# Kernel optimization log

Measured on AMD Instinct MI355X. Metric: run time of the kernel, lower is better.

Reference implementation:

```python
import jax, jax.numpy as jnp
import numpy as np

N = 100000
E = 1600000
GENE = 512
HID = 128
NCLS = 10
EPS = 1e-5  # BatchNorm1d default eps


def setup_inputs() -> dict:
    key = jax.random.key(0)
    ks = jax.random.split(key, 16)
    def lin(k, fan_in, fan_out):
        return (jax.random.normal(k, (fan_in, fan_out), jnp.float32) / np.sqrt(fan_in)).astype(jnp.float32)
    dims = [(GENE, HID), (HID, 2 * HID), (2 * HID, HID), (HID, HID // 2)]
    inp = {}
    inp["x"] = jax.random.normal(ks[0], (N, GENE), jnp.float32)
    inp["edge_index"] = jax.random.randint(ks[1], (2, E), 0, N)
    for i, (di, do) in enumerate(dims, start=1):
        inp[f"W{i}"] = lin(ks[1 + i], di, do)
        inp[f"b{i}"] = jnp.zeros((do,), jnp.float32)
        inp[f"g{i}"] = jnp.ones((do,), jnp.float32)     # BN gamma
        inp[f"beta{i}"] = jnp.zeros((do,), jnp.float32)  # BN beta
    inp["Wc"] = lin(ks[10], HID // 2, NCLS)
    inp["bc"] = jnp.zeros((NCLS,), jnp.float32)
    return inp


def gcn_conv(h_in, W, b, src, dst, deg_inv_sqrt):
    # PyG GCNConv: transform, then symmetric-normalized aggregation with self-loops
    h = h_in @ W                                   # [N, out]
    norm = (deg_inv_sqrt[src] * deg_inv_sqrt[dst])[:, None]  # [E, 1]
    agg = jnp.zeros_like(h).at[dst].add(h[src] * norm)       # scatter-add over edges
    agg = agg + h * (deg_inv_sqrt ** 2)[:, None]   # self-loop contribution (norm = 1/deg)
    return agg + b


def relu_bn(h, g, beta):
    # forward applies BatchNorm1d(F.relu(h)) in training mode (batch stats, biased var)
    h = jax.nn.relu(h)
    mu = h.mean(axis=0)
    var = h.var(axis=0)
    return (h - mu) * jax.lax.rsqrt(var + EPS) * g + beta


def reference(x, edge_index, W1, b1, g1, beta1, W2, b2, g2, beta2,
              W3, b3, g3, beta3, W4, b4, g4, beta4, Wc, bc):
    src, dst = edge_index[0], edge_index[1]
    # degree after adding self-loops (edge weight 1)
    deg = jnp.zeros((x.shape[0],), x.dtype).at[dst].add(1.0) + 1.0
    dis = jax.lax.rsqrt(deg)
    h = relu_bn(gcn_conv(x, W1, b1, src, dst, dis), g1, beta1)
    h = relu_bn(gcn_conv(h, W2, b2, src, dst, dis), g2, beta2)
    h = relu_bn(gcn_conv(h, W3, b3, src, dst, dis), g3, beta3)
    h = relu_bn(gcn_conv(h, W4, b4, src, dst, dis), g4, beta4)
    return h @ Wc + bc
```

## Files before the change

kernel.cpp:

```cpp
#include <hip/hip_runtime.h>
#include <hip/hip_bf16.h>

#define EPS_BN 1e-5f

using frag8 = __attribute__((ext_vector_type(8))) short;
using f32x4 = __attribute__((ext_vector_type(4))) float;

typedef const __attribute__((address_space(1))) void* gas_ptr;
typedef __attribute__((address_space(3))) void* las_ptr;

__device__ __forceinline__ void async_ld16(const void* g, void* l) {
  __builtin_amdgcn_global_load_lds((gas_ptr)g, (las_ptr)l, 16, 0, 0);
}

__device__ __forceinline__ float bfu2f(unsigned short u) {
  union { unsigned int i; float f; } c;
  c.i = (unsigned int)u << 16;
  return c.f;
}

__global__ __launch_bounds__(256) void prep_fat_kernel(
    const int* __restrict__ e_dst, int* __restrict__ cnt, int* __restrict__ rank, int E,
    int CB,
    const float* __restrict__ x, __hip_bfloat16* __restrict__ Xb, size_t n4, int VB,
    const float* __restrict__ W1, const float* __restrict__ W2,
    const float* __restrict__ W3, const float* __restrict__ W4,
    __hip_bfloat16* __restrict__ T1, __hip_bfloat16* __restrict__ T2,
    __hip_bfloat16* __restrict__ T3, __hip_bfloat16* __restrict__ T4) {
  int b = (int)blockIdx.x;
  int tid = (int)threadIdx.x;
  if (b < CB) {
    int e = b * 256 + tid;
    if (e < E) rank[e] = atomicAdd(&cnt[e_dst[e]], 1);
  } else if (b < CB + VB) {
    size_t i = (size_t)(b - CB) * 256 + tid;
    size_t stride = (size_t)VB * 256;
    for (; i < n4; i += stride) {
      float4 v = *(const float4*)&x[i * 4];
      union { ushort4 u; __hip_bfloat16 h[4]; } pk;
      pk.h[0] = __float2bfloat16(v.x);
      pk.h[1] = __float2bfloat16(v.y);
      pk.h[2] = __float2bfloat16(v.z);
      pk.h[3] = __float2bfloat16(v.w);
      *(ushort4*)&Xb[i * 4] = pk.u;
    }
  } else {
    int i = (b - CB - VB) * 256 + tid;
    const float* W; __hip_bfloat16* T; int F, K, base;
    if (i < 65536)        { W = W1; T = T1; K = 512; F = 128; base = 0; }
    else if (i < 98304)   { W = W2; T = T2; K = 128; F = 256; base = 65536; }
    else if (i < 131072)  { W = W3; T = T3; K = 256; F = 128; base = 98304; }
    else if (i < 139264)  { W = W4; T = T4; K = 128; F = 64;  base = 131072; }
    else return;
    int j = i - base;
    int k = j / F, f = j % F;
    T[f * K + k] = __float2bfloat16(W[j]);
  }
}

__global__ void scan1_kernel(const int* __restrict__ cnt, int* __restrict__ out,
                             int* __restrict__ bsum, float* __restrict__ dis, int n) {
  __shared__ int sdata[1024];
  int tid = threadIdx.x;
  int i = blockIdx.x * 1024 + tid;
  int v = (i < n) ? cnt[i] : 0;
  if (i < n) dis[i] = rsqrtf((float)v + 1.0f);
  sdata[tid] = v;
  __syncthreads();
  for (int off = 1; off < 1024; off <<= 1) {
    int t = (tid >= off) ? sdata[tid - off] : 0;
    __syncthreads();
    sdata[tid] += t;
    __syncthreads();
  }
  if (i < n) out[i] = sdata[tid] - v;
  if (tid == 1023) bsum[blockIdx.x] = sdata[1023];
}

__global__ void scan2_kernel(int* __restrict__ bsum, int nb) {
  __shared__ int sdata[1024];
  int tid = threadIdx.x;
  int v = (tid < nb) ? bsum[tid] : 0;
  sdata[tid] = v;
  __syncthreads();
  for (int off = 1; off < 1024; off <<= 1) {
    int t = (tid >= off) ? sdata[tid - off] : 0;
    __syncthreads();
    sdata[tid] += t;
    __syncthreads();
  }
  if (tid < nb) bsum[tid] = sdata[tid] - v;
}

__global__ void scan3_kernel(int* __restrict__ out, const int* __restrict__ bsum,
                             int n, int E) {
  int i = blockIdx.x * 1024 + threadIdx.x;
  if (i < n) out[i] += bsum[blockIdx.x];
  if (i == 0) out[n] = E;
}

template <int TN, int OMODE>
__device__ __forceinline__ void gemm_body(
    const __hip_bfloat16* __restrict__ A, const __hip_bfloat16* __restrict__ Bt,
    void* __restrict__ Cv, const float* __restrict__ bias,
    const float* __restrict__ rowscale, float* __restrict__ stats,
    int Nr, int K, int F, int bx, int by) {
  constexpr int WM = (TN == 128) ? 64 : 32;
  constexpr int MI = WM / 16;
  __shared__ __align__(16) __hip_bfloat16 As[128 * 32];
  __shared__ __align__(16) __hip_bfloat16 Bs[TN * 32];
  __shared__ float sacc[128], sqc[128];
  int tid = (int)threadIdx.x;
  int wid = tid >> 6, lane = tid & 63;
  int rowBase = bx * 128;
  int colBase = by * TN;
  int wr, wc;
  if (TN == 128) { wr = (wid >> 1) * 64; wc = (wid & 1) * 64; }
  else           { wr = wid * 32;        wc = 0; }

  f32x4 zero = {0.f, 0.f, 0.f, 0.f};
  f32x4 acc[MI][4];
#pragma unroll
  for (int i = 0; i < MI; ++i)
#pragma unroll
    for (int j = 0; j < 4; ++j) acc[i][j] = zero;

  int lm = lane & 15;
  int k8 = (lane >> 4) * 8;

  if constexpr (OMODE == 2) {
    if (tid < 128) { sacc[tid] = 0.f; sqc[tid] = 0.f; }
  }

  for (int k0 = 0; k0 < K; k0 += 32) {
#pragma unroll
    for (int p = 0; p < 2; ++p) {
      int sidx = p * 256 + tid;
      int row = sidx >> 2;
      int kq = (sidx & 3) * 8;
      int gr = rowBase + row;
      if (gr >= Nr) gr = Nr - 1;
      async_ld16(A + (size_t)gr * K + k0 + kq, (char*)As + (p * 256 + wid * 64) * 16);
    }
    constexpr int BPASS = TN / 64;
#pragma unroll
    for (int p = 0; p < BPASS; ++p) {
      int sidx = p * 256 + tid;
      int col = sidx >> 2;
      int kq = (sidx & 3) * 8;
      async_ld16(Bt + (size_t)(colBase + col) * K + k0 + kq,
                 (char*)Bs + (p * 256 + wid * 64) * 16);
    }
    __syncthreads();

    frag8 af[MI], bf[4];
#pragma unroll
    for (int i = 0; i < MI; ++i)
      af[i] = *(const frag8*)&As[(wr + i * 16 + lm) * 32 + k8];
#pragma unroll
    for (int j = 0; j < 4; ++j)
      bf[j] = *(const frag8*)&Bs[(wc + j * 16 + lm) * 32 + k8];
#pragma unroll
    for (int i = 0; i < MI; ++i)
#pragma unroll
      for (int j = 0; j < 4; ++j)
        acc[i][j] = __builtin_amdgcn_mfma_f32_16x16x32_bf16(af[i], bf[j], acc[i][j], 0, 0, 0);
    __syncthreads();
  }

  int rquad = (lane >> 4) * 4;
  float s[4] = {0.f, 0.f, 0.f, 0.f}, q[4] = {0.f, 0.f, 0.f, 0.f};
#pragma unroll
  for (int i = 0; i < MI; ++i) {
    int rb = rowBase + wr + i * 16 + rquad;
#pragma unroll
    for (int r = 0; r < 4; ++r) {
      int row = rb + r;
      if (row < Nr) {
        if constexpr (OMODE == 1) {
          float rs = rowscale[row];
#pragma unroll
          for (int j = 0; j < 4; ++j) {
            int col = colBase + wc + j * 16 + lm;
            ((__hip_bfloat16*)Cv)[(size_t)row * F + col] = __float2bfloat16(acc[i][j][r] * rs);
          }
        } else {
#pragma unroll
          for (int j = 0; j < 4; ++j) {
            int col = colBase + wc + j * 16 + lm;
            float v = acc[i][j][r] + bias[col];
            ((float*)Cv)[(size_t)row * F + col] = v;
            float rl = fmaxf(v, 0.f);
            s[j] += rl;
            q[j] += rl * rl;
          }
        }
      }
    }
  }

  if constexpr (OMODE == 2) {
#pragma unroll
    for (int j = 0; j < 4; ++j) {
      s[j] += __shfl_xor(s[j], 16, 64); s[j] += __shfl_xor(s[j], 32, 64);
      q[j] += __shfl_xor(q[j], 16, 64); q[j] += __shfl_xor(q[j], 32, 64);
    }
    if (lane < 16) {
#pragma unroll
      for (int j = 0; j < 4; ++j) {
        atomicAdd(&sacc[wc + j * 16 + lane], s[j]);
        atomicAdd(&sqc[wc + j * 16 + lane], q[j]);
      }
    }
    __syncthreads();
    if (tid < 128) {
      atomicAdd(&stats[colBase + tid], sacc[tid]);
      atomicAdd(&stats[256 + colBase + tid], sqc[tid]);
    }
  }
}

template <int TN, int OMODE>
__global__ __launch_bounds__(256) void mfma_gemm_kernel(
    const __hip_bfloat16* __restrict__ A, const __hip_bfloat16* __restrict__ Bt,
    void* __restrict__ Cv, const float* __restrict__ bias,
    const float* __restrict__ rowscale, float* __restrict__ stats,
    int Nr, int K, int F) {
  gemm_body<TN, OMODE>(A, Bt, Cv, bias, rowscale, stats, Nr, K, F,
                       (int)blockIdx.x, (int)blockIdx.y);
}

__global__ __launch_bounds__(256) void gemm1_scatter_kernel(
    const __hip_bfloat16* __restrict__ A, const __hip_bfloat16* __restrict__ Bt,
    void* __restrict__ Cv, const float* __restrict__ rowscale,
    int Nr, int K, int F, int G1,
    const int* __restrict__ src, const int* __restrict__ dst,
    const int* __restrict__ rowstart, const int* __restrict__ rank,
    int* __restrict__ csr_src, int E) {
  int b = (int)blockIdx.x;
  if (b < G1) {
    gemm_body<128, 1>(A, Bt, Cv, nullptr, rowscale, nullptr, Nr, K, F, b, 0);
  } else {
    int e = (b - G1) * 256 + (int)threadIdx.x;
    if (e < E) csr_src[rowstart[dst[e]] + rank[e]] = src[e];
  }
}

template <int VEC, int OMODE>
__global__ __launch_bounds__(256) void agg_kernel(
    const __hip_bfloat16* __restrict__ Ts, const int* __restrict__ rowstart,
    const int* __restrict__ csr_src, const float* __restrict__ dis,
    const float* __restrict__ bias, void* __restrict__ H,
    float* __restrict__ stats, int Nn, int F) {
  __shared__ float lsum[512], lqs[512];
  int tid = (int)threadIdx.x;
  int wid4 = tid >> 6;
  int lane = tid & 63;
  int off = lane * VEC;
  const unsigned short* Tu = (const unsigned short*)Ts;

  float bj[VEC];
  float s[VEC], q[VEC];
#pragma unroll
  for (int j = 0; j < VEC; ++j) {
    bj[j] = (OMODE == 1) ? bias[off + j] : 0.f;
    s[j] = 0.f; q[j] = 0.f;
  }

  for (int d = blockIdx.x * 4 + wid4; d < Nn; d += gridDim.x * 4) {
    float acc[VEC];
    {
      unsigned short r[VEC];
      if constexpr (VEC == 2) *(ushort2*)r = *(const ushort2*)&Tu[(size_t)d * F + off];
      else                    r[0] = Tu[(size_t)d * F + off];
#pragma unroll
      for (int j = 0; j < VEC; ++j) acc[j] = bfu2f(r[j]);
    }

    int e0 = rowstart[d], e1 = rowstart[d + 1];
    for (int e = e0; e < e1; e += 16) {
      int idx[16];
      bool val[16];
#pragma unroll
      for (int p = 0; p < 16; ++p) {
        int ee = e + p;
        val[p] = ee < e1;
        idx[p] = csr_src[val[p] ? ee : e1 - 1];
      }
      unsigned short r[16][VEC];
#pragma unroll
      for (int p = 0; p < 16; ++p) {
        if constexpr (VEC == 2) *(ushort2*)r[p] = *(const ushort2*)&Tu[(size_t)idx[p] * F + off];
        else                    r[p][0] = Tu[(size_t)idx[p] * F + off];
      }
#pragma unroll
      for (int p = 0; p < 16; ++p)
#pragma unroll
        for (int j = 0; j < VEC; ++j) acc[j] += val[p] ? bfu2f(r[p][j]) : 0.f;
    }

    float dd = dis[d];
    if constexpr (OMODE == 0) {
      union { ushort2 u; __hip_bfloat16 h[2]; } pk;
      if constexpr (VEC == 2) {
        pk.h[0] = __float2bfloat16(acc[0] * dd);
        pk.h[1] = __float2bfloat16(acc[1] * dd);
        *(ushort2*)&((__hip_bfloat16*)H)[(size_t)d * F + off] = pk.u;
      } else {
        ((__hip_bfloat16*)H)[(size_t)d * F + off] = __float2bfloat16(acc[0] * dd);
      }
    } else {
      float v[VEC];
#pragma unroll
      for (int j = 0; j < VEC; ++j) {
        v[j] = acc[j] * dd + bj[j];
        float rl = fmaxf(v[j], 0.f);
        s[j] += rl;
        q[j] += rl * rl;
      }
      if constexpr (VEC == 2) {
        *(float2*)&((float*)H)[(size_t)d * F + off] = make_float2(v[0], v[1]);
      } else {
        ((float*)H)[(size_t)d * F + off] = v[0];
      }
    }
  }

  if constexpr (OMODE == 1) {
#pragma unroll
    for (int j = 0; j < VEC; ++j) {
      lsum[(lane * VEC + j) * 4 + wid4] = s[j];
      lqs[(lane * VEC + j) * 4 + wid4] = q[j];
    }
    __syncthreads();
    int nc = 64 * VEC;
    for (int c = tid; c < nc; c += 256) {
      float a = lsum[c * 4 + 0] + lsum[c * 4 + 1] + lsum[c * 4 + 2] + lsum[c * 4 + 3];
      float b = lqs[c * 4 + 0] + lqs[c * 4 + 1] + lqs[c * 4 + 2] + lqs[c * 4 + 3];
      atomicAdd(&stats[c], a);
      atomicAdd(&stats[256 + c], b);
    }
  }
}

__global__ __launch_bounds__(256) void bnapply_kernel(
    const float* __restrict__ H, const float* __restrict__ stats,
    const float* __restrict__ g, const float* __restrict__ beta,
    const float* __restrict__ rowscale, __hip_bfloat16* __restrict__ O,
    size_t total4, int F, int logF, float invN) {
  __shared__ float ssc[256], ssb[256];
  int tid = (int)threadIdx.x;
  if (tid < F) {
    float mean = stats[tid] * invN;
    float var = stats[256 + tid] * invN - mean * mean;
    float sc = g[tid] * rsqrtf(var + EPS_BN);
    ssc[tid] = sc;
    ssb[tid] = beta[tid] - mean * sc;
  }
  __syncthreads();
  size_t i = (size_t)blockIdx.x * blockDim.x + tid;
  size_t stride = (size_t)gridDim.x * blockDim.x;
  for (; i < total4; i += stride) {
    size_t b = i * 4;
    float4 v = *(const float4*)&H[b];
    int c = (int)(b & (size_t)(F - 1));
    float rs = rowscale ? rowscale[b >> logF] : 1.0f;
    union { ushort4 u; __hip_bfloat16 h[4]; } pk;
    pk.h[0] = __float2bfloat16((fmaxf(v.x, 0.f) * ssc[c + 0] + ssb[c + 0]) * rs);
    pk.h[1] = __float2bfloat16((fmaxf(v.y, 0.f) * ssc[c + 1] + ssb[c + 1]) * rs);
    pk.h[2] = __float2bfloat16((fmaxf(v.z, 0.f) * ssc[c + 2] + ssb[c + 2]) * rs);
    pk.h[3] = __float2bfloat16((fmaxf(v.w, 0.f) * ssc[c + 3] + ssb[c + 3]) * rs);
    *(ushort4*)&O[b] = pk.u;
  }
}

__global__ __launch_bounds__(256) void bnapply_cls_kernel(
    const float* __restrict__ Hf, const float* __restrict__ stats,
    const float* __restrict__ g, const float* __restrict__ beta,
    const float* __restrict__ Wc, const float* __restrict__ bc,
    float* __restrict__ out, int Nn, float invN) {
  __shared__ float ssc[64], ssb[64];
  int tid = (int)threadIdx.x;
  if (tid < 64) {
    float mean = stats[tid] * invN;
    float var = stats[256 + tid] * invN - mean * mean;
    float sc = g[tid] * rsqrtf(var + EPS_BN);
    ssc[tid] = sc;
    ssb[tid] = beta[tid] - mean * sc;
  }
  __syncthreads();
  int gt = blockIdx.x * blockDim.x + tid;
  int wid = gt >> 6;
  int lane = tid & 63;
  if (wid >= Nn) return;
  float v = Hf[(size_t)wid * 64 + lane];
  float h = fmaxf(v, 0.f) * ssc[lane] + ssb[lane];
#pragma unroll
  for (int c = 0; c < 10; ++c) {
    float p = h * Wc[lane * 10 + c];
#pragma unroll
    for (int off = 32; off > 0; off >>= 1) p += __shfl_down(p, off, 64);
    if (lane == 0) out[(size_t)wid * 10 + c] = p + bc[c];
  }
}


extern "C" void kernel_launch(void* const* d_in, const int* in_sizes, int n_in,
                              void* d_out, int out_size, void* d_ws, size_t ws_size,
                              hipStream_t stream) {
  (void)n_in; (void)out_size; (void)ws_size;
  const float* x    = (const float*)d_in[0];
  const int*   edge = (const int*)d_in[1];
  const int E  = in_sizes[1] / 2;
  const int Nn = in_sizes[0] / 512;
  const int* e_src = edge;
  const int* e_dst = edge + E;

  const float* W[4]  = {(const float*)d_in[2],  (const float*)d_in[6],
                        (const float*)d_in[10], (const float*)d_in[14]};
  const float* bv[4] = {(const float*)d_in[3],  (const float*)d_in[7],
                        (const float*)d_in[11], (const float*)d_in[15]};
  const float* gv[4] = {(const float*)d_in[4],  (const float*)d_in[8],
                        (const float*)d_in[12], (const float*)d_in[16]};
  const float* bt[4] = {(const float*)d_in[5],  (const float*)d_in[9],
                        (const float*)d_in[13], (const float*)d_in[17]};
  const float* Wc = (const float*)d_in[18];
  const float* bc = (const float*)d_in[19];
  float* out = (float*)d_out;

  const int Kdim[4] = {512, 128, 256, 128};
  const int Fdim[4] = {128, 256, 128, 64};
  const float invN = 1.0f / (float)Nn;

  char* p = (char*)d_ws;
  auto alloc = [&](size_t bytes) -> void* {
    void* r = (void*)p;
    p += (bytes + 255) & ~(size_t)255;
    return r;
  };
  int*   cnt      = (int*)alloc((size_t)Nn * 4);
  float* stats    = (float*)alloc(2048 * 4);
  size_t zeroBytes = (size_t)(((size_t)Nn * 4 + 255) & ~(size_t)255) + 2048 * 4;
  int*   rowstart = (int*)alloc((size_t)(Nn + 1) * 4);
  int*   bsum     = (int*)alloc(1024 * 4);
  float* dis      = (float*)alloc((size_t)Nn * 4);
  int*   rank     = (int*)alloc((size_t)E * 4);
  int*   csr_src  = (int*)alloc((size_t)E * 4);
  __hip_bfloat16* Wt[4];
  for (int l = 0; l < 4; ++l)
    Wt[l] = (__hip_bfloat16*)alloc((size_t)Kdim[l] * Fdim[l] * 2);
  char* R0 = (char*)alloc((size_t)Nn * 512 * 2);
  __hip_bfloat16* Tb = (__hip_bfloat16*)alloc((size_t)Nn * 256 * 2);
  __hip_bfloat16* P0 = (__hip_bfloat16*)alloc((size_t)Nn * 256 * 2);
  __hip_bfloat16* P1 = (__hip_bfloat16*)alloc((size_t)Nn * 256 * 2);
  __hip_bfloat16* Xb = (__hip_bfloat16*)R0;
  float*          Hf = (float*)R0;

  hipMemsetAsync(cnt, 0, zeroBytes, stream);

  const int CB = (E + 255) / 256;
  const int VB = 2048;
  const int WB = (139264 + 255) / 256;
  prep_fat_kernel<<<CB + VB + WB, 256, 0, stream>>>(
      e_dst, cnt, rank, E, CB,
      x, Xb, (size_t)Nn * 512 / 4, VB,
      W[0], W[1], W[2], W[3], Wt[0], Wt[1], Wt[2], Wt[3]);

  int nb = (Nn + 1023) / 1024;
  scan1_kernel<<<nb, 1024, 0, stream>>>(cnt, rowstart, bsum, dis, Nn);
  scan2_kernel<<<1, 1024, 0, stream>>>(bsum, nb);
  scan3_kernel<<<nb, 1024, 0, stream>>>(rowstart, bsum, Nn, E);

  const int AGG_BLOCKS = 1536;
  int gx = (Nn + 127) / 128;

  gemm1_scatter_kernel<<<gx + CB, 256, 0, stream>>>(
      Xb, Wt[0], Tb, dis, Nn, 512, 128, gx,
      e_src, e_dst, rowstart, rank, csr_src, E);
  agg_kernel<2, 1><<<AGG_BLOCKS, 256, 0, stream>>>(Tb, rowstart, csr_src, dis,
                                                   bv[0], Hf, stats, Nn, 128);
  bnapply_kernel<<<(int)(((size_t)Nn * 128 / 4 + 255) / 256), 256, 0, stream>>>(
      Hf, stats, gv[0], bt[0], dis, P0, (size_t)Nn * 128 / 4, 128, 7, invN);

  agg_kernel<2, 0><<<AGG_BLOCKS, 256, 0, stream>>>(P0, rowstart, csr_src, dis,
                                                   nullptr, Tb, nullptr, Nn, 128);
  {
    dim3 g(gx, 2);
    mfma_gemm_kernel<128, 2><<<g, 256, 0, stream>>>(Tb, Wt[1], Hf, bv[1], nullptr,
                                                    stats + 512, Nn, 128, 256);
  }
  bnapply_kernel<<<(int)(((size_t)Nn * 256 / 4 + 255) / 256), 256, 0, stream>>>(
      Hf, stats + 512, gv[1], bt[1], nullptr, P1, (size_t)Nn * 256 / 4, 256, 8, invN);

  {
    dim3 g(gx, 1);
    mfma_gemm_kernel<128, 1><<<g, 256, 0, stream>>>(P1, Wt[2], Tb, nullptr, dis, nullptr,
                                                    Nn, 256, 128);
  }
  agg_kernel<2, 1><<<AGG_BLOCKS, 256, 0, stream>>>(Tb, rowstart, csr_src, dis,
                                                   bv[2], Hf, stats + 1024, Nn, 128);
  bnapply_kernel<<<(int)(((size_t)Nn * 128 / 4 + 255) / 256), 256, 0, stream>>>(
      Hf, stats + 1024, gv[2], bt[2], nullptr, P0, (size_t)Nn * 128 / 4, 128, 7, invN);

  {
    dim3 g(gx, 1);
    mfma_gemm_kernel<64, 1><<<g, 256, 0, stream>>>(P0, Wt[3], Tb, nullptr, dis, nullptr,
                                                   Nn, 128, 64);
  }
  agg_kernel<1, 1><<<AGG_BLOCKS, 256, 0, stream>>>(Tb, rowstart, csr_src, dis,
                                                   bv[3], Hf, stats + 1536, Nn, 64);
  int clsBlocks = (Nn * 64 + 255) / 256;
  bnapply_cls_kernel<<<clsBlocks, 256, 0, stream>>>(Hf, stats + 1536, gv[3], bt[3],
                                                    Wc, bc, out, Nn, invN);
}
```

Baseline: 1.040 ms.

## Fuse BatchNorm apply into aggregation and GEMM loaders, drop standalone BN passes

Removes the separate bnapply kernels by folding the BN affine transform into the next consumer: the layer-2 aggregation uses a per-node sum of neighbour norms so the affine can be applied after summation, and the GEMM A-loaders apply scale and shift while staging tiles. Layer 1 now reads fp32 x directly in the GEMM, with an in-register bf16 conversion, instead of a separate conversion pass. Row scaling by dis is moved into a fused scatter kernel. Intermediates are stored as bf16 ReLU outputs rather than fp32 pre-activations. This cuts memory traffic and launch count, but the synchronous A-loads replace async LDS loads and the GEMM runs before the CSR build, which changes rounding and the overlap pattern.

```diff
diff --git a/kernel.cpp b/kernel.cpp
--- a/kernel.cpp
+++ b/kernel.cpp
@@ -19,42 +19,12 @@
   return c.f;
 }
 
-__global__ __launch_bounds__(256) void prep_fat_kernel(
-    const int* __restrict__ e_dst, int* __restrict__ cnt, int* __restrict__ rank, int E,
-    int CB,
-    const float* __restrict__ x, __hip_bfloat16* __restrict__ Xb, size_t n4, int VB,
-    const float* __restrict__ W1, const float* __restrict__ W2,
-    const float* __restrict__ W3, const float* __restrict__ W4,
-    __hip_bfloat16* __restrict__ T1, __hip_bfloat16* __restrict__ T2,
-    __hip_bfloat16* __restrict__ T3, __hip_bfloat16* __restrict__ T4) {
-  int b = (int)blockIdx.x;
-  int tid = (int)threadIdx.x;
-  if (b < CB) {
-    int e = b * 256 + tid;
-    if (e < E) rank[e] = atomicAdd(&cnt[e_dst[e]], 1);
-  } else if (b < CB + VB) {
-    size_t i = (size_t)(b - CB) * 256 + tid;
-    size_t stride = (size_t)VB * 256;
-    for (; i < n4; i += stride) {
-      float4 v = *(const float4*)&x[i * 4];
-      union { ushort4 u; __hip_bfloat16 h[4]; } pk;
-      pk.h[0] = __float2bfloat16(v.x);
-      pk.h[1] = __float2bfloat16(v.y);
-      pk.h[2] = __float2bfloat16(v.z);
-      pk.h[3] = __float2bfloat16(v.w);
-      *(ushort4*)&Xb[i * 4] = pk.u;
-    }
-  } else {
-    int i = (b - CB - VB) * 256 + tid;
-    const float* W; __hip_bfloat16* T; int F, K, base;
-    if (i < 65536)        { W = W1; T = T1; K = 512; F = 128; base = 0; }
-    else if (i < 98304)   { W = W2; T = T2; K = 128; F = 256; base = 65536; }
-    else if (i < 131072)  { W = W3; T = T3; K = 256; F = 128; base = 98304; }
-    else if (i < 139264)  { W = W4; T = T4; K = 128; F = 64;  base = 131072; }
-    else return;
-    int j = i - base;
-    int k = j / F, f = j % F;
-    T[f * K + k] = __float2bfloat16(W[j]);
+
+__global__ void wtrans1_kernel(const float* __restrict__ W1, __hip_bfloat16* __restrict__ T) {
+  int i = blockIdx.x * blockDim.x + threadIdx.x;
+  if (i < 512 * 128) {
+    int k = i / 128, f = i % 128;
+    T[f * 512 + k] = __float2bfloat16(W1[i]);
   }
 }
 
@@ -99,17 +69,20 @@
   if (i == 0) out[n] = E;
 }
 
-template <int TN, int OMODE>
+template <int TN, int ASTAGE, int OMODE>
 __device__ __forceinline__ void gemm_body(
-    const __hip_bfloat16* __restrict__ A, const __hip_bfloat16* __restrict__ Bt,
-    void* __restrict__ Cv, const float* __restrict__ bias,
-    const float* __restrict__ rowscale, float* __restrict__ stats,
+    const void* __restrict__ Ap, const __hip_bfloat16* __restrict__ Bt,
+    __hip_bfloat16* __restrict__ C, const float* __restrict__ bias,
+    const float* __restrict__ rowscale,
+    const float* __restrict__ statsIn, const float* __restrict__ g,
+    const float* __restrict__ beta, float* __restrict__ statsOut, float invN,
     int Nr, int K, int F, int bx, int by) {
   constexpr int WM = (TN == 128) ? 64 : 32;
   constexpr int MI = WM / 16;
   __shared__ __align__(16) __hip_bfloat16 As[128 * 32];
   __shared__ __align__(16) __hip_bfloat16 Bs[TN * 32];
   __shared__ float sacc[128], sqc[128];
+  __shared__ float ssc[256], ssb[256];
   int tid = (int)threadIdx.x;
   int wid = tid >> 6, lane = tid & 63;
   int rowBase = bx * 128;
@@ -128,19 +101,65 @@
   int lm = lane & 15;
   int k8 = (lane >> 4) * 8;
 
-  if constexpr (OMODE == 2) {
+  if constexpr (OMODE == 3) {
     if (tid < 128) { sacc[tid] = 0.f; sqc[tid] = 0.f; }
   }
+  if constexpr (ASTAGE == 2) {
+    for (int k = tid; k < K; k += 256) {
+      float mean = statsIn[k] * invN;
+      float var = statsIn[256 + k] * invN - mean * mean;
+      float sc = g[k] * rsqrtf(var + EPS_BN);
+      ssc[k] = sc;
+      ssb[k] = beta[k] - mean * sc;
+    }
+    __syncthreads();
+  }
 
   for (int k0 = 0; k0 < K; k0 += 32) {
-#pragma unroll
-    for (int p = 0; p < 2; ++p) {
-      int sidx = p * 256 + tid;
-      int row = sidx >> 2;
-      int kq = (sidx & 3) * 8;
-      int gr = rowBase + row;
-      if (gr >= Nr) gr = Nr - 1;
-      async_ld16(A + (size_t)gr * K + k0 + kq, (char*)As + (p * 256 + wid * 64) * 16);
+    if constexpr (ASTAGE == 0) {
+#pragma unroll
+      for (int p = 0; p < 2; ++p) {
+        int sidx = p * 256 + tid;
+        int row = sidx >> 2;
+        int kq = (sidx & 3) * 8;
+        int gr = rowBase + row;
+        if (gr >= Nr) gr = Nr - 1;
+        async_ld16((const __hip_bfloat16*)Ap + (size_t)gr * K + k0 + kq,
+                   (char*)As + (p * 256 + wid * 64) * 16);
+      }
+    } else {
+#pragma unroll
+      for (int p = 0; p < 2; ++p) {
+        int sidx = p * 256 + tid;
+        int row = sidx >> 2;
+        int kq = (sidx & 3) * 8;
+        int gr = rowBase + row;
+        if (gr >= Nr) gr = Nr - 1;
+        union { frag8 f; __hip_bfloat16 h[8]; } pk;
+        if constexpr (ASTAGE == 1) {
+          const float* s = (const float*)Ap + (size_t)gr * K + k0 + kq;
+          float4 a = *(const float4*)s;
+          float4 b2 = *(const float4*)(s + 4);
+          pk.h[0] = __float2bfloat16(a.x);  pk.h[1] = __float2bfloat16(a.y);
+          pk.h[2] = __float2bfloat16(a.z);  pk.h[3] = __float2bfloat16(a.w);
+          pk.h[4] = __float2bfloat16(b2.x); pk.h[5] = __float2bfloat16(b2.y);
+          pk.h[6] = __float2bfloat16(b2.z); pk.h[7] = __float2bfloat16(b2.w);
+        } else {
+          const unsigned short* s = (const unsigned short*)Ap + (size_t)gr * K + k0 + kq;
+          ushort4 a = *(const ushort4*)s;
+          ushort4 b2 = *(const ushort4*)(s + 4);
+          int kk = k0 + kq;
+          pk.h[0] = __float2bfloat16(bfu2f(a.x)  * ssc[kk + 0] + ssb[kk + 0]);
+          pk.h[1] = __float2bfloat16(bfu2f(a.y)  * ssc[kk + 1] + ssb[kk + 1]);
+          pk.h[2] = __float2bfloat16(bfu2f(a.z)  * ssc[kk + 2] + ssb[kk + 2]);
+          pk.h[3] = __float2bfloat16(bfu2f(a.w)  * ssc[kk + 3] + ssb[kk + 3]);
+          pk.h[4] = __float2bfloat16(bfu2f(b2.x) * ssc[kk + 4] + ssb[kk + 4]);
+          pk.h[5] = __float2bfloat16(bfu2f(b2.y) * ssc[kk + 5] + ssb[kk + 5]);
+          pk.h[6] = __float2bfloat16(bfu2f(b2.z) * ssc[kk + 6] + ssb[kk + 6]);
+          pk.h[7] = __float2bfloat16(bfu2f(b2.w) * ssc[kk + 7] + ssb[kk + 7]);
+        }
+        *(frag8*)&As[row * 32 + kq] = pk.f;
+      }
     }
     constexpr int BPASS = TN / 64;
 #pragma unroll
@@ -177,20 +196,26 @@
     for (int r = 0; r < 4; ++r) {
       int row = rb + r;
       if (row < Nr) {
-        if constexpr (OMODE == 1) {
-          float rs = rowscale[row];
+        if constexpr (OMODE == 0) {
 #pragma unroll
           for (int j = 0; j < 4; ++j) {
             int col = colBase + wc + j * 16 + lm;
-            ((__hip_bfloat16*)Cv)[(size_t)row * F + col] = __float2bfloat16(acc[i][j][r] * rs);
+            C[(size_t)row * F + col] = __float2bfloat16(acc[i][j][r]);
+          }
+        } else if constexpr (OMODE == 1) {
+          float rs = rowscale[row];
+#pragma unroll
+          for (int j = 0; j < 4; ++j) {
+            int col = colBase + wc + j * 16 + lm;
+            C[(size_t)row * F + col] = __float2bfloat16(acc[i][j][r] * rs);
           }
         } else {
 #pragma unroll
           for (int j = 0; j < 4; ++j) {
             int col = colBase + wc + j * 16 + lm;
             float v = acc[i][j][r] + bias[col];
-            ((float*)Cv)[(size_t)row * F + col] = v;
             float rl = fmaxf(v, 0.f);
+            C[(size_t)row * F + col] = __float2bfloat16(rl);
             s[j] += rl;
             q[j] += rl * rl;
           }
@@ -199,7 +224,7 @@
     }
   }
 
-  if constexpr (OMODE == 2) {
+  if constexpr (OMODE == 3) {
 #pragma unroll
     for (int j = 0; j < 4; ++j) {
       s[j] += __shfl_xor(s[j], 16, 64); s[j] += __shfl_xor(s[j], 32, 64);
@@ -214,56 +239,114 @@
     }
     __syncthreads();
     if (tid < 128) {
-      atomicAdd(&stats[colBase + tid], sacc[tid]);
-      atomicAdd(&stats[256 + colBase + tid], sqc[tid]);
-    }
-  }
-}
-
-template <int TN, int OMODE>
+      atomicAdd(&statsOut[colBase + tid], sacc[tid]);
+      atomicAdd(&statsOut[256 + colBase + tid], sqc[tid]);
+    }
+  }
+}
+
+__global__ __launch_bounds__(256) void fat1_kernel(
+    const float* __restrict__ x, const __hip_bfloat16* __restrict__ Wt0,
+    __hip_bfloat16* __restrict__ T1, int Nn, int G1,
+    const int* __restrict__ e_dst, int* __restrict__ cnt, int* __restrict__ rank,
+    int E, int CB,
+    const float* __restrict__ W2, const float* __restrict__ W3, const float* __restrict__ W4,
+    __hip_bfloat16* __restrict__ Tw2, __hip_bfloat16* __restrict__ Tw3,
+    __hip_bfloat16* __restrict__ Tw4) {
+  int b = (int)blockIdx.x;
+  if (b < G1) {
+    gemm_body<128, 1, 0>(x, Wt0, T1, nullptr, nullptr, nullptr, nullptr, nullptr,
+                         nullptr, 0.f, Nn, 512, 128, b, 0);
+  } else if (b < G1 + CB) {
+    int e = (b - G1) * 256 + (int)threadIdx.x;
+    if (e < E) rank[e] = atomicAdd(&cnt[e_dst[e]], 1);
+  } else {
+    int i = (b - G1 - CB) * 256 + (int)threadIdx.x;
+    const float* W; __hip_bfloat16* T; int K, F, base;
+    if (i < 32768)       { W = W2; T = Tw2; K = 128; F = 256; base = 0; }
+    else if (i < 65536)  { W = W3; T = Tw3; K = 256; F = 128; base = 32768; }
+    else if (i < 73728)  { W = W4; T = Tw4; K = 128; F = 64;  base = 65536; }
+    else return;
+    int j = i - base;
+    int k = j / F, f = j % F;
+    T[f * K + k] = __float2bfloat16(W[j]);
+  }
+}
+
+template <int TN, int ASTAGE, int OMODE>
 __global__ __launch_bounds__(256) void mfma_gemm_kernel(
-    const __hip_bfloat16* __restrict__ A, const __hip_bfloat16* __restrict__ Bt,
-    void* __restrict__ Cv, const float* __restrict__ bias,
-    const float* __restrict__ rowscale, float* __restrict__ stats,
-    int Nr, int K, int F) {
-  gemm_body<TN, OMODE>(A, Bt, Cv, bias, rowscale, stats, Nr, K, F,
-                       (int)blockIdx.x, (int)blockIdx.y);
-}
-
-__global__ __launch_bounds__(256) void gemm1_scatter_kernel(
-    const __hip_bfloat16* __restrict__ A, const __hip_bfloat16* __restrict__ Bt,
-    void* __restrict__ Cv, const float* __restrict__ rowscale,
-    int Nr, int K, int F, int G1,
+    const void* __restrict__ A, const __hip_bfloat16* __restrict__ Bt,
+    __hip_bfloat16* __restrict__ C, const float* __restrict__ bias,
+    const float* __restrict__ rowscale, const float* __restrict__ statsIn,
+    const float* __restrict__ g, const float* __restrict__ beta,
+    float* __restrict__ statsOut, float invN, int Nr, int K, int F) {
+  gemm_body<TN, ASTAGE, OMODE>(A, Bt, C, bias, rowscale, statsIn, g, beta, statsOut,
+                               invN, Nr, K, F, (int)blockIdx.x, (int)blockIdx.y);
+}
+
+__global__ __launch_bounds__(256) void fat2_kernel(
     const int* __restrict__ src, const int* __restrict__ dst,
     const int* __restrict__ rowstart, const int* __restrict__ rank,
-    int* __restrict__ csr_src, int E) {
+    int* __restrict__ csr_src, int E, int SB,
+    __hip_bfloat16* __restrict__ T1, const float* __restrict__ dis, int n8) {
   int b = (int)blockIdx.x;
-  if (b < G1) {
-    gemm_body<128, 1>(A, Bt, Cv, nullptr, rowscale, nullptr, Nr, K, F, b, 0);
+  if (b < SB) {
+    int e = b * 256 + (int)threadIdx.x;
+    if (e < E) csr_src[rowstart[dst[e]] + rank[e]] = src[e];
   } else {
-    int e = (b - G1) * 256 + (int)threadIdx.x;
-    if (e < E) csr_src[rowstart[dst[e]] + rank[e]] = src[e];
-  }
-}
-
-template <int VEC, int OMODE>
+    int i = (b - SB) * 256 + (int)threadIdx.x;
+    if (i < n8) {
+      float dd = dis[i >> 4];
+      unsigned short* p8 = (unsigned short*)T1 + (size_t)i * 8;
+      ushort4 a = *(ushort4*)p8;
+      ushort4 c = *(ushort4*)(p8 + 4);
+      union { ushort4 u; __hip_bfloat16 h[4]; } o0, o1;
+      o0.h[0] = __float2bfloat16(bfu2f(a.x) * dd);
+      o0.h[1] = __float2bfloat16(bfu2f(a.y) * dd);
+      o0.h[2] = __float2bfloat16(bfu2f(a.z) * dd);
+      o0.h[3] = __float2bfloat16(bfu2f(a.w) * dd);
+      o1.h[0] = __float2bfloat16(bfu2f(c.x) * dd);
+      o1.h[1] = __float2bfloat16(bfu2f(c.y) * dd);
+      o1.h[2] = __float2bfloat16(bfu2f(c.z) * dd);
+      o1.h[3] = __float2bfloat16(bfu2f(c.w) * dd);
+      *(ushort4*)p8 = o0.u;
+      *(ushort4*)(p8 + 4) = o1.u;
+    }
+  }
+}
+
+template <int VEC, int AMODE>
 __global__ __launch_bounds__(256) void agg_kernel(
     const __hip_bfloat16* __restrict__ Ts, const int* __restrict__ rowstart,
     const int* __restrict__ csr_src, const float* __restrict__ dis,
     const float* __restrict__ bias, void* __restrict__ H,
-    float* __restrict__ stats, int Nn, int F) {
+    float* __restrict__ stats, const float* __restrict__ statsIn,
+    const float* __restrict__ g, const float* __restrict__ beta,
+    float* __restrict__ sd, float invN, int Nn, int F) {
   __shared__ float lsum[512], lqs[512];
+  __shared__ float ssc[128], ssb[128];
   int tid = (int)threadIdx.x;
   int wid4 = tid >> 6;
   int lane = tid & 63;
   int off = lane * VEC;
   const unsigned short* Tu = (const unsigned short*)Ts;
 
+  if constexpr (AMODE == 2) {
+    if (tid < F) {
+      float mean = statsIn[tid] * invN;
+      float var = statsIn[256 + tid] * invN - mean * mean;
+      float sc = g[tid] * rsqrtf(var + EPS_BN);
+      ssc[tid] = sc;
+      ssb[tid] = beta[tid] - mean * sc;
+    }
+    __syncthreads();
+  }
+
   float bj[VEC];
   float s[VEC], q[VEC];
 #pragma unroll
   for (int j = 0; j < VEC; ++j) {
-    bj[j] = (OMODE == 1) ? bias[off + j] : 0.f;
+    bj[j] = (AMODE == 1 || AMODE == 3 || AMODE == 4) ? bias[off + j] : 0.f;
     s[j] = 0.f; q[j] = 0.f;
   }
 
@@ -276,6 +359,8 @@
 #pragma unroll
       for (int j = 0; j < VEC; ++j) acc[j] = bfu2f(r[j]);
     }
+    float dd = dis[d];
+    float sdacc = dd;
 
     int e0 = rowstart[d], e1 = rowstart[d + 1];
     for (int e = e0; e < e1; e += 16) {
@@ -288,45 +373,54 @@
         idx[p] = csr_src[val[p] ? ee : e1 - 1];
       }
       unsigned short r[16][VEC];
+      float dv[16];
 #pragma unroll
       for (int p = 0; p < 16; ++p) {
         if constexpr (VEC == 2) *(ushort2*)r[p] = *(const ushort2*)&Tu[(size_t)idx[p] * F + off];
         else                    r[p][0] = Tu[(size_t)idx[p] * F + off];
-      }
-#pragma unroll
-      for (int p = 0; p < 16; ++p)
+        if constexpr (AMODE == 1) dv[p] = dis[idx[p]];
+      }
+#pragma unroll
+      for (int p = 0; p < 16; ++p) {
 #pragma unroll
         for (int j = 0; j < VEC; ++j) acc[j] += val[p] ? bfu2f(r[p][j]) : 0.f;
-    }
-
-    float dd = dis[d];
-    if constexpr (OMODE == 0) {
+        if constexpr (AMODE == 1) sdacc += val[p] ? dv[p] : 0.f;
+      }
+    }
+
+    if constexpr (AMODE == 2) {
+      float sdv = sd[d];
       union { ushort2 u; __hip_bfloat16 h[2]; } pk;
-      if constexpr (VEC == 2) {
-        pk.h[0] = __float2bfloat16(acc[0] * dd);
-        pk.h[1] = __float2bfloat16(acc[1] * dd);
+      pk.h[0] = __float2bfloat16(dd * (ssc[off + 0] * acc[0] + ssb[off + 0] * sdv));
+      pk.h[1] = __float2bfloat16(dd * (ssc[off + 1] * acc[1] + ssb[off + 1] * sdv));
+      *(ushort2*)&((__hip_bfloat16*)H)[(size_t)d * F + off] = pk.u;
+    } else {
+      float rl[VEC];
+#pragma unroll
+      for (int j = 0; j < VEC; ++j) {
+        float v = acc[j] * dd + bj[j];
+        rl[j] = fmaxf(v, 0.f);
+        s[j] += rl[j];
+        q[j] += rl[j] * rl[j];
+      }
+      if constexpr (AMODE == 1) {
+        union { ushort2 u; __hip_bfloat16 h[2]; } pk;
+        pk.h[0] = __float2bfloat16(rl[0] * dd);
+        pk.h[1] = __float2bfloat16(rl[1] * dd);
+        *(ushort2*)&((__hip_bfloat16*)H)[(size_t)d * F + off] = pk.u;
+        if (lane == 0) sd[d] = sdacc;
+      } else if constexpr (AMODE == 3) {
+        union { ushort2 u; __hip_bfloat16 h[2]; } pk;
+        pk.h[0] = __float2bfloat16(rl[0]);
+        pk.h[1] = __float2bfloat16(rl[1]);
         *(ushort2*)&((__hip_bfloat16*)H)[(size_t)d * F + off] = pk.u;
       } else {
-        ((__hip_bfloat16*)H)[(size_t)d * F + off] = __float2bfloat16(acc[0] * dd);
-      }
-    } else {
-      float v[VEC];
-#pragma unroll
-      for (int j = 0; j < VEC; ++j) {
-        v[j] = acc[j] * dd + bj[j];
-        float rl = fmaxf(v[j], 0.f);
-        s[j] += rl;
-        q[j] += rl * rl;
-      }
-      if constexpr (VEC == 2) {
-        *(float2*)&((float*)H)[(size_t)d * F + off] = make_float2(v[0], v[1]);
-      } else {
-        ((float*)H)[(size_t)d * F + off] = v[0];
-      }
-    }
-  }
-
-  if constexpr (OMODE == 1) {
+        ((float*)H)[(size_t)d * F + off] = rl[0];
+      }
+    }
+  }
+
+  if constexpr (AMODE != 2) {
 #pragma unroll
     for (int j = 0; j < VEC; ++j) {
       lsum[(lane * VEC + j) * 4 + wid4] = s[j];
@@ -343,39 +437,8 @@
   }
 }
 
-__global__ __launch_bounds__(256) void bnapply_kernel(
-    const float* __restrict__ H, const float* __restrict__ stats,
-    const float* __restrict__ g, const float* __restrict__ beta,
-    const float* __restrict__ rowscale, __hip_bfloat16* __restrict__ O,
-    size_t total4, int F, int logF, float invN) {
-  __shared__ float ssc[256], ssb[256];
-  int tid = (int)threadIdx.x;
-  if (tid < F) {
-    float mean = stats[tid] * invN;
-    float var = stats[256 + tid] * invN - mean * mean;
-    float sc = g[tid] * rsqrtf(var + EPS_BN);
-    ssc[tid] = sc;
-    ssb[tid] = beta[tid] - mean * sc;
-  }
-  __syncthreads();
-  size_t i = (size_t)blockIdx.x * blockDim.x + tid;
-  size_t stride = (size_t)gridDim.x * blockDim.x;
-  for (; i < total4; i += stride) {
-    size_t b = i * 4;
-    float4 v = *(const float4*)&H[b];
-    int c = (int)(b & (size_t)(F - 1));
-    float rs = rowscale ? rowscale[b >> logF] : 1.0f;
-    union { ushort4 u; __hip_bfloat16 h[4]; } pk;
-    pk.h[0] = __float2bfloat16((fmaxf(v.x, 0.f) * ssc[c + 0] + ssb[c + 0]) * rs);
-    pk.h[1] = __float2bfloat16((fmaxf(v.y, 0.f) * ssc[c + 1] + ssb[c + 1]) * rs);
-    pk.h[2] = __float2bfloat16((fmaxf(v.z, 0.f) * ssc[c + 2] + ssb[c + 2]) * rs);
-    pk.h[3] = __float2bfloat16((fmaxf(v.w, 0.f) * ssc[c + 3] + ssb[c + 3]) * rs);
-    *(ushort4*)&O[b] = pk.u;
-  }
-}
-
 __global__ __launch_bounds__(256) void bnapply_cls_kernel(
-    const float* __restrict__ Hf, const float* __restrict__ stats,
+    const float* __restrict__ R4, const float* __restrict__ stats,
     const float* __restrict__ g, const float* __restrict__ beta,
     const float* __restrict__ Wc, const float* __restrict__ bc,
     float* __restrict__ out, int Nn, float invN) {
@@ -393,8 +456,8 @@
   int wid = gt >> 6;
   int lane = tid & 63;
   if (wid >= Nn) return;
-  float v = Hf[(size_t)wid * 64 + lane];
-  float h = fmaxf(v, 0.f) * ssc[lane] + ssb[lane];
+  float v = R4[(size_t)wid * 64 + lane];
+  float h = v * ssc[lane] + ssb[lane];
 #pragma unroll
   for (int c = 0; c < 10; ++c) {
     float p = h * Wc[lane * 10 + c];
@@ -428,8 +491,6 @@
   const float* bc = (const float*)d_in[19];
   float* out = (float*)d_out;
 
-  const int Kdim[4] = {512, 128, 256, 128};
-  const int Fdim[4] = {128, 256, 128, 64};
   const float invN = 1.0f / (float)Nn;
 
   char* p = (char*)d_ws;
@@ -444,72 +505,76 @@
   int*   rowstart = (int*)alloc((size_t)(Nn + 1) * 4);
   int*   bsum     = (int*)alloc(1024 * 4);
   float* dis      = (float*)alloc((size_t)Nn * 4);
+  float* sd       = (float*)alloc((size_t)Nn * 4);
   int*   rank     = (int*)alloc((size_t)E * 4);
   int*   csr_src  = (int*)alloc((size_t)E * 4);
-  __hip_bfloat16* Wt[4];
-  for (int l = 0; l < 4; ++l)
-    Wt[l] = (__hip_bfloat16*)alloc((size_t)Kdim[l] * Fdim[l] * 2);
-  char* R0 = (char*)alloc((size_t)Nn * 512 * 2);
-  __hip_bfloat16* Tb = (__hip_bfloat16*)alloc((size_t)Nn * 256 * 2);
-  __hip_bfloat16* P0 = (__hip_bfloat16*)alloc((size_t)Nn * 256 * 2);
-  __hip_bfloat16* P1 = (__hip_bfloat16*)alloc((size_t)Nn * 256 * 2);
-  __hip_bfloat16* Xb = (__hip_bfloat16*)R0;
-  float*          Hf = (float*)R0;
+  __hip_bfloat16* Wt0 = (__hip_bfloat16*)alloc(512 * 128 * 2);
+  __hip_bfloat16* Wt1 = (__hip_bfloat16*)alloc(128 * 256 * 2);
+  __hip_bfloat16* Wt2 = (__hip_bfloat16*)alloc(256 * 128 * 2);
+  __hip_bfloat16* Wt3 = (__hip_bfloat16*)alloc(128 * 64 * 2);
+  __hip_bfloat16* Ts1 = (__hip_bfloat16*)alloc((size_t)Nn * 128 * 2);
+  __hip_bfloat16* R1  = (__hip_bfloat16*)alloc((size_t)Nn * 128 * 2);
+  __hip_bfloat16* Tb2 = (__hip_bfloat16*)alloc((size_t)Nn * 128 * 2);
+  __hip_bfloat16* R2  = (__hip_bfloat16*)alloc((size_t)Nn * 256 * 2);
+  __hip_bfloat16* Ts3 = (__hip_bfloat16*)alloc((size_t)Nn * 128 * 2);
+  __hip_bfloat16* R3  = (__hip_bfloat16*)alloc((size_t)Nn * 128 * 2);
+  __hip_bfloat16* Ts4 = (__hip_bfloat16*)alloc((size_t)Nn * 64 * 2);
+  float*          R4  = (float*)alloc((size_t)Nn * 64 * 4);
 
   hipMemsetAsync(cnt, 0, zeroBytes, stream);
 
+  wtrans1_kernel<<<(512 * 128 + 255) / 256, 256, 0, stream>>>(W[0], Wt0);
+
+  const int gx = (Nn + 127) / 128;
   const int CB = (E + 255) / 256;
-  const int VB = 2048;
-  const int WB = (139264 + 255) / 256;
-  prep_fat_kernel<<<CB + VB + WB, 256, 0, stream>>>(
-      e_dst, cnt, rank, E, CB,
-      x, Xb, (size_t)Nn * 512 / 4, VB,
-      W[0], W[1], W[2], W[3], Wt[0], Wt[1], Wt[2], Wt[3]);
+  const int WB = (73728 + 255) / 256;
+  fat1_kernel<<<gx + CB + WB, 256, 0, stream>>>(
+      x, Wt0, Ts1, Nn, gx, e_dst, cnt, rank, E, CB,
+      W[1], W[2], W[3], Wt1, Wt2, Wt3);
 
   int nb = (Nn + 1023) / 1024;
   scan1_kernel<<<nb, 1024, 0, stream>>>(cnt, rowstart, bsum, dis, Nn);
   scan2_kernel<<<1, 1024, 0, stream>>>(bsum, nb);
   scan3_kernel<<<nb, 1024, 0, stream>>>(rowstart, bsum, Nn, E);
 
-  const int AGG_BLOCKS = 1536;
-  int gx = (Nn + 127) / 128;
-
-  gemm1_scatter_kernel<<<gx + CB, 256, 0, stream>>>(
-      Xb, Wt[0], Tb, dis, Nn, 512, 128, gx,
-      e_src, e_dst, rowstart, rank, csr_src, E);
-  agg_kernel<2, 1><<<AGG_BLOCKS, 256, 0, stream>>>(Tb, rowstart, csr_src, dis,
-                                                   bv[0], Hf, stats, Nn, 128);
-  bnapply_kernel<<<(int)(((size_t)Nn * 128 / 4 + 255) / 256), 256, 0, stream>>>(
-      Hf, stats, gv[0], bt[0], dis, P0, (size_t)Nn * 128 / 4, 128, 7, invN);
-
-  agg_kernel<2, 0><<<AGG_BLOCKS, 256, 0, stream>>>(P0, rowstart, csr_src, dis,
-                                                   nullptr, Tb, nullptr, Nn, 128);
+  int n8 = Nn * 128 / 8;
+  int TB = (n8 + 255) / 256;
+  fat2_kernel<<<CB + TB, 256, 0, stream>>>(e_src, e_dst, rowstart, rank, csr_src, E, CB,
+                                           Ts1, dis, n8);
+
+  const int AGG_BLOCKS = 2048;
+
+  agg_kernel<2, 1><<<AGG_BLOCKS, 256, 0, stream>>>(
+      Ts1, rowstart, csr_src, dis, bv[0], R1, stats, nullptr, nullptr, nullptr,
+      sd, invN, Nn, 128);
+  agg_kernel<2, 2><<<AGG_BLOCKS, 256, 0, stream>>>(
+      R1, rowstart, csr_src, dis, nullptr, Tb2, nullptr, stats, gv[0], bt[0],
+      sd, invN, Nn, 128);
   {
     dim3 g(gx, 2);
-    mfma_gemm_kernel<128, 2><<<g, 256, 0, stream>>>(Tb, Wt[1], Hf, bv[1], nullptr,
-                                                    stats + 512, Nn, 128, 256);
-  }
-  bnapply_kernel<<<(int)(((size_t)Nn * 256 / 4 + 255) / 256), 256, 0, stream>>>(
-      Hf, stats + 512, gv[1], bt[1], nullptr, P1, (size_t)Nn * 256 / 4, 256, 8, invN);
-
+    mfma_gemm_kernel<128, 0, 3><<<g, 256, 0, stream>>>(
+        Tb2, Wt1, R2, bv[1], nullptr, nullptr, nullptr, nullptr, stats + 512, invN,
+        Nn, 128, 256);
+  }
   {
     dim3 g(gx, 1);
-    mfma_gemm_kernel<128, 1><<<g, 256, 0, stream>>>(P1, Wt[2], Tb, nullptr, dis, nullptr,
-                                                    Nn, 256, 128);
-  }
-  agg_kernel<2, 1><<<AGG_BLOCKS, 256, 0, stream>>>(Tb, rowstart, csr_src, dis,
-                                                   bv[2], Hf, stats + 1024, Nn, 128);
-  bnapply_kernel<<<(int)(((size_t)Nn * 128 / 4 + 255) / 256), 256, 0, stream>>>(
-      Hf, stats + 1024, gv[2], bt[2], nullptr, P0, (size_t)Nn * 128 / 4, 128, 7, invN);
-
+    mfma_gemm_kernel<128, 2, 1><<<g, 256, 0, stream>>>(
+        R2, Wt2, Ts3, nullptr, dis, stats + 512, gv[1], bt[1], nullptr, invN,
+        Nn, 256, 128);
+  }
+  agg_kernel<2, 3><<<AGG_BLOCKS, 256, 0, stream>>>(
+      Ts3, rowstart, csr_src, dis, bv[2], R3, stats + 1024, nullptr, nullptr, nullptr,
+      nullptr, invN, Nn, 128);
   {
     dim3 g(gx, 1);
-    mfma_gemm_kernel<64, 1><<<g, 256, 0, stream>>>(P0, Wt[3], Tb, nullptr, dis, nullptr,
-                                                   Nn, 128, 64);
-  }
-  agg_kernel<1, 1><<<AGG_BLOCKS, 256, 0, stream>>>(Tb, rowstart, csr_src, dis,
-                                                   bv[3], Hf, stats + 1536, Nn, 64);
+    mfma_gemm_kernel<64, 2, 1><<<g, 256, 0, stream>>>(
+        R3, Wt3, Ts4, nullptr, dis, stats + 1024, gv[2], bt[2], nullptr, invN,
+        Nn, 128, 64);
+  }
+  agg_kernel<1, 4><<<AGG_BLOCKS, 256, 0, stream>>>(
+      Ts4, rowstart, csr_src, dis, bv[3], R4, stats + 1536, nullptr, nullptr, nullptr,
+      nullptr, invN, Nn, 64);
   int clsBlocks = (Nn * 64 + 255) / 256;
-  bnapply_cls_kernel<<<clsBlocks, 256, 0, stream>>>(Hf, stats + 1536, gv[3], bt[3],
+  bnapply_cls_kernel<<<clsBlocks, 256, 0, stream>>>(R4, stats + 1536, gv[3], bt[3],
                                                     Wc, bc, out, Nn, invN);
 }
```

Result: faster. 950.0 us (-8.7%).
